# Optimization experiments

Measured on AMD Instinct MI355X. Metric: run time of the kernel, lower is better.

Reference implementation:

```python
import jax, jax.numpy as jnp
import numpy as np

B, S, H, D = 2, 2048, 16, 128
HID = H * D  # 2048


def _quantum(x, real, imag, phase, mag):
    # |x * e^{i*phase} * (real + i*imag) * mag| == |x| * sqrt(real^2+imag^2) * |mag|
    # (phase has unit modulus, so it drops out of the magnitude; grad wrt phase is 0,
    # matching torch.abs of the complex product.)
    return jnp.abs(x) * jnp.sqrt(real * real + imag * imag) * jnp.abs(mag)


def setup_inputs() -> dict:
    key = jax.random.key(0)
    ks = jax.random.split(key, 20)
    p = lambda i, shape, s=0.02: jax.random.normal(ks[i], shape, dtype=jnp.float32) * s
    inp = {
        "hidden_states": jax.random.normal(ks[0], (B, S, HID), dtype=jnp.float32),
        "attention_mask": jnp.zeros((B, 1, 1, S), dtype=jnp.float32),
    }
    i = 1
    for name in ("q", "k", "v"):
        inp[name + "_real"] = p(i, (HID,)); i += 1
        inp[name + "_imag"] = p(i, (HID,)); i += 1
        inp[name + "_phase"] = p(i, (HID,), 0.1); i += 1
        inp[name + "_mag"] = jnp.ones((HID,), dtype=jnp.float32)
    for name in ("q", "k", "v", "o"):
        inp["W" + name] = p(i, (HID, HID)); i += 1  # torch Linear weight [out, in]
        inp["b" + name] = jnp.zeros((HID,), dtype=jnp.float32)
    inp["ent"] = p(i, (H, H))
    return inp


def reference(hidden_states, attention_mask,
              q_real, q_imag, q_phase, q_mag,
              k_real, k_imag, k_phase, k_mag,
              v_real, v_imag, v_phase, v_mag,
              Wq, bq, Wk, bk, Wv, bv, Wo, bo, ent):
    Bsz, Sl, _ = hidden_states.shape

    def heads(x):  # [B,S,HID] -> [B,H,S,D]
        return x.reshape(Bsz, Sl, H, D).transpose(0, 2, 1, 3)

    q = heads(_quantum(hidden_states @ Wq.T + bq, q_real, q_imag, q_phase, q_mag))
    k = heads(_quantum(hidden_states @ Wk.T + bk, k_real, k_imag, k_phase, k_mag))
    v = heads(_quantum(hidden_states @ Wv.T + bv, v_real, v_imag, v_phase, v_mag))

    scores = jnp.einsum('bhsd,bhtd->bhst', q, k) / jnp.sqrt(jnp.float32(D))
    # entanglement bias: [H,H] tiled along key axis -> [1,H,1,S]
    bias = jnp.tile(ent, (1, Sl // H))[None, :, None, :]
    scores = scores + bias + attention_mask
    probs = jax.nn.softmax(scores, axis=-1)

    ctx = jnp.einsum('bhst,bhtd->bhsd', probs, v)
    ctx = ctx.transpose(0, 2, 1, 3).reshape(Bsz, Sl, HID)
    return ctx @ Wo.T + bo
```

## Files before the change

kernel.cpp:

```cpp
#include <hip/hip_runtime.h>
#include <hip/hip_bf16.h>

#define NB 2
#define NS 2048
#define NH 16
#define ND 128
#define HID2 2048
#define MROWS 4096

typedef __bf16 bf16;
typedef bf16 bf16x8 __attribute__((ext_vector_type(8)));
typedef bf16 bf16x4 __attribute__((ext_vector_type(4)));
typedef float f32x4 __attribute__((ext_vector_type(4)));
typedef unsigned int u32;

#define GLOBAL_AS __attribute__((address_space(1)))
#define LDS_AS __attribute__((address_space(3)))

__device__ __forceinline__ void async16(void* lds, const void* g) {
    __builtin_amdgcn_global_load_lds((const GLOBAL_AS u32*)g, (LDS_AS u32*)lds, 16, 0, 0);
}

__global__ void cvt_f32_bf16(const float* __restrict__ src, bf16* __restrict__ dst, int n8) {
    int i = blockIdx.x * blockDim.x + threadIdx.x;
    if (i >= n8) return;
    const float4* s4 = (const float4*)src;
    float4 a = s4[2 * i], b = s4[2 * i + 1];
    bf16x8 o;
    o[0] = (bf16)a.x; o[1] = (bf16)a.y; o[2] = (bf16)a.z; o[3] = (bf16)a.w;
    o[4] = (bf16)b.x; o[5] = (bf16)b.y; o[6] = (bf16)b.z; o[7] = (bf16)b.w;
    ((bf16x8*)dst)[i] = o;
}

__global__ void cvt_w4(const float* __restrict__ Wq, const float* __restrict__ Wk,
                       const float* __restrict__ Wv, const float* __restrict__ Wo,
                       bf16* __restrict__ dst) {
    int z = blockIdx.y;
    const float* src = (z == 0) ? Wq : (z == 1) ? Wk : (z == 2) ? Wv : Wo;
    int i = blockIdx.x * blockDim.x + threadIdx.x;
    const float4* s4 = (const float4*)src;
    float4 a = s4[2 * i], b = s4[2 * i + 1];
    bf16x8 o;
    o[0] = (bf16)a.x; o[1] = (bf16)a.y; o[2] = (bf16)a.z; o[3] = (bf16)a.w;
    o[4] = (bf16)b.x; o[5] = (bf16)b.y; o[6] = (bf16)b.z; o[7] = (bf16)b.w;
    ((bf16x8*)(dst + (size_t)z * HID2 * HID2))[i] = o;
}

__global__ void qscale_kernel(const float* qr, const float* qi, const float* qm,
                              const float* kr, const float* ki, const float* km,
                              const float* vr, const float* vi, const float* vm,
                              float* out) {
    int i = blockIdx.x * blockDim.x + threadIdx.x;
    if (i >= HID2) return;
    out[i]            = sqrtf(qr[i] * qr[i] + qi[i] * qi[i]) * fabsf(qm[i]);
    out[HID2 + i]     = sqrtf(kr[i] * kr[i] + ki[i] * ki[i]) * fabsf(km[i]);
    out[2 * HID2 + i] = sqrtf(vr[i] * vr[i] + vi[i] * vi[i]) * fabsf(vm[i]);
}

__device__ __forceinline__ void stage6(const char* gA, const char* gB,
                                       char* sa, char* sb, int w, int lane) {
#pragma unroll
    for (int j = 0; j < 2; ++j) {
        int r = w * 16 + j * 8 + (lane >> 3);
        async16(sa + (w * 16 + j * 8) * 128,
                gA + (size_t)r * (HID2 * 2) + (((lane & 7) * 16) ^ ((r & 7) << 4)));
    }
#pragma unroll
    for (int j = 0; j < 4; ++j) {
        int r = w * 32 + j * 8 + (lane >> 3);
        async16(sb + (w * 32 + j * 8) * 128,
                gB + (size_t)r * (HID2 * 2) + (((lane & 7) * 16) ^ ((r & 7) << 4)));
    }
}

template <int MODE>
__device__ __forceinline__ void gemm8_core(const bf16* __restrict__ A, const bf16* __restrict__ Bt,
                                           const float* __restrict__ bias, const float* __restrict__ scale,
                                           void* __restrict__ Cout, int tm, int tn) {
    __shared__ bf16 sA[3][128 * 64];
    __shared__ bf16 sB[3][256 * 64];
    const int NT = HID2 / 64;
    int tid = threadIdx.x, w = tid >> 6, lane = tid & 63;
    int wr = w >> 2, wc = w & 3;
    int l15 = lane & 15, l4 = lane >> 4;
    int xorb = (l15 & 7) << 4;

    const char* gAb = (const char*)(A + (size_t)tm * 128 * HID2);
    const char* gBb = (const char*)(Bt + (size_t)tn * 256 * HID2);

    f32x4 acc[4][4] = {};

    stage6(gAb, gBb, (char*)sA[0], (char*)sB[0], w, lane);
    stage6(gAb + 128, gBb + 128, (char*)sA[1], (char*)sB[1], w, lane);
    asm volatile("s_waitcnt vmcnt(6)" ::: "memory");
    __builtin_amdgcn_s_barrier();
    asm volatile("" ::: "memory");

    int cur = 0, nxt = 2;
    for (int t = 0; t < NT; ++t) {
        const char* pa = (const char*)sA[cur];
        const char* pb = (const char*)sB[cur];
        if (t + 2 < NT)
            stage6(gAb + (size_t)(t + 2) * 128, gBb + (size_t)(t + 2) * 128,
                   (char*)sA[nxt], (char*)sB[nxt], w, lane);
#pragma unroll
        for (int kk = 0; kk < 2; ++kk) {
            bf16x8 af[4], bg[4];
#pragma unroll
            for (int m = 0; m < 4; ++m)
                af[m] = *(const bf16x8*)(pa + (wr * 64 + m * 16 + l15) * 128 + ((kk * 64 + l4 * 16) ^ xorb));
#pragma unroll
            for (int n = 0; n < 4; ++n)
                bg[n] = *(const bf16x8*)(pb + (wc * 64 + n * 16 + l15) * 128 + ((kk * 64 + l4 * 16) ^ xorb));
#pragma unroll
            for (int m = 0; m < 4; ++m)
#pragma unroll
                for (int n = 0; n < 4; ++n)
                    acc[m][n] = __builtin_amdgcn_mfma_f32_16x16x32_bf16(af[m], bg[n], acc[m][n], 0, 0, 0);
        }
        if (t + 2 < NT)       { asm volatile("s_waitcnt vmcnt(6)" ::: "memory"); }
        else if (t + 2 == NT) { asm volatile("s_waitcnt vmcnt(0)" ::: "memory"); }
        if (t + 1 < NT) {
            __builtin_amdgcn_s_barrier();
            asm volatile("" ::: "memory");
        }
        cur = (cur == 2) ? 0 : cur + 1;
        nxt = (nxt == 2) ? 0 : nxt + 1;
    }

#pragma unroll
    for (int n = 0; n < 4; ++n) {
        int col = tn * 256 + wc * 64 + n * 16 + l15;
        float bv = bias[col];
        float sc = (MODE == 0) ? scale[col] : 0.f;
#pragma unroll
        for (int m = 0; m < 4; ++m) {
            int row = tm * 128 + wr * 64 + m * 16 + l4 * 4;
            if (MODE == 0) {
                bf16* Cp = (bf16*)Cout;
#pragma unroll
                for (int r = 0; r < 4; ++r)
                    Cp[(size_t)(row + r) * HID2 + col] = (bf16)(fabsf(acc[m][n][r] + bv) * sc);
            } else {
                float* Cp = (float*)Cout;
#pragma unroll
                for (int r = 0; r < 4; ++r)
                    Cp[(size_t)(row + r) * HID2 + col] = acc[m][n][r] + bv;
            }
        }
    }
}

__global__ __launch_bounds__(512, 2) void gemm8_qkv(
    const bf16* __restrict__ X, const bf16* __restrict__ Wb,
    const float* __restrict__ bq, const float* __restrict__ bk, const float* __restrict__ bv,
    const float* __restrict__ scales, bf16* __restrict__ QKV) {
    int z = blockIdx.y;
    int bid = blockIdx.x;
    int tn = bid & 7, tm = bid >> 3;
    const bf16* W = Wb + (size_t)z * HID2 * HID2;
    const float* bias = (z == 0) ? bq : (z == 1) ? bk : bv;
    gemm8_core<0>(X, W, bias, scales + z * HID2, QKV + (size_t)z * MROWS * HID2, tm, tn);
}

__global__ __launch_bounds__(512, 2) void gemm8_out(
    const bf16* __restrict__ Ctx, const bf16* __restrict__ Wo,
    const float* __restrict__ bo, float* __restrict__ out) {
    int bid = blockIdx.x;
    int tn = bid & 7, tm = bid >> 3;
    gemm8_core<1>(Ctx, Wo, bo, nullptr, out, tm, tn);
}

__global__ void transpose_v(const bf16* __restrict__ Vb, bf16* __restrict__ Vt) {
    int bh = blockIdx.z;
    int b = bh >> 4, h = bh & 15;
    int s0 = blockIdx.x * 64, d0 = blockIdx.y * 64;
    int tid = threadIdx.x;
    __shared__ bf16 T[64][72];
    const bf16* src = Vb + ((size_t)b * NS + s0) * HID2 + h * ND + d0;
#pragma unroll
    for (int i = 0; i < 2; ++i) {
        int r = i * 32 + (tid >> 3);
        int c = (tid & 7) * 8;
        *(bf16x8*)(&T[r][c]) = *(const bf16x8*)(src + (size_t)r * HID2 + c);
    }
    __syncthreads();
    bf16* dst = Vt + ((size_t)(b * NH + h) * ND + d0) * NS + s0;
#pragma unroll
    for (int i = 0; i < 2; ++i) {
        int dr = i * 32 + (tid >> 3);
        int sc = (tid & 7) * 8;
        bf16x8 o;
#pragma unroll
        for (int j = 0; j < 8; ++j) o[j] = T[sc + j][dr];
        *(bf16x8*)(dst + (size_t)dr * NS + sc) = o;
    }
}

__device__ __forceinline__ void stage_load(const bf16* __restrict__ Kp, const bf16* __restrict__ Vp,
                                           int kt, int tid, bf16x8 kreg[4], bf16x8 vreg[4]) {
#pragma unroll
    for (int i = 0; i < 4; ++i) {
        kreg[i] = *(const bf16x8*)(Kp + (size_t)(kt * 64 + i * 16 + (tid >> 4)) * HID2 + (tid & 15) * 8);
        vreg[i] = *(const bf16x8*)(Vp + (size_t)(i * 32 + (tid >> 3)) * NS + kt * 64 + (tid & 7) * 8);
    }
}

__global__ __launch_bounds__(256, 2) void flash_kernel(
    const bf16* __restrict__ Qb, const bf16* __restrict__ Kb, const bf16* __restrict__ Vt,
    const float* __restrict__ ent, const float* __restrict__ mask, bf16* __restrict__ Ctx) {
    int qt = blockIdx.x;
    int bh = blockIdx.y;
    int b = bh >> 4, h = bh & 15;
    int tid = threadIdx.x, wid = tid >> 6, lane = tid & 63;
    int l15 = lane & 15, l4 = lane >> 4;

    __shared__ bf16 Ks[64 * 136];
    __shared__ bf16 Vs[128 * 72];
    __shared__ bf16 Ps[4][32 * 72];

    const bf16* Qp = Qb + ((size_t)b * NS + qt * 128) * HID2 + h * ND;
    const bf16* Kp = Kb + (size_t)b * NS * HID2 + h * ND;
    const bf16* Vp = Vt + (size_t)(b * NH + h) * ND * NS;
    const float* maskp = mask + (size_t)b * NS;

    bf16x8 qf[2][4];
#pragma unroll
    for (int m = 0; m < 2; ++m)
#pragma unroll
        for (int kk = 0; kk < 4; ++kk)
            qf[m][kk] = *(const bf16x8*)(Qp + (size_t)(wid * 32 + m * 16 + l15) * HID2 + kk * 32 + l4 * 8);

    float eb[4];
#pragma unroll
    for (int r = 0; r < 4; ++r) eb[r] = ent[h * NH + l4 * 4 + r];
    const float RSQD = 0.08838834764831845f;

    float mrun[2], lrun[2];
    mrun[0] = mrun[1] = -INFINITY;
    lrun[0] = lrun[1] = 0.f;
    f32x4 oacc[2][8] = {};

    bf16x8 kreg[4], vreg[4];
    stage_load(Kp, Vp, 0, tid, kreg, vreg);
#pragma unroll
    for (int i = 0; i < 4; ++i) {
        *(bf16x8*)(&Ks[(i * 16 + (tid >> 4)) * 136 + (tid & 15) * 8]) = kreg[i];
        *(bf16x8*)(&Vs[(i * 32 + (tid >> 3)) * 72 + (tid & 7) * 8]) = vreg[i];
    }

    for (int kt = 0; kt < NS / 64; ++kt) {
        __syncthreads();
        if (kt + 1 < NS / 64) stage_load(Kp, Vp, kt + 1, tid, kreg, vreg);

        f32x4 s[2][4] = {};
#pragma unroll
        for (int kk = 0; kk < 4; ++kk) {
            bf16x8 kf[4];
#pragma unroll
            for (int n = 0; n < 4; ++n)
                kf[n] = *(const bf16x8*)(&Ks[(n * 16 + l15) * 136 + kk * 32 + l4 * 8]);
#pragma unroll
            for (int m = 0; m < 2; ++m)
#pragma unroll
                for (int n = 0; n < 4; ++n)
                    s[m][n] = __builtin_amdgcn_mfma_f32_16x16x32_bf16(kf[n], qf[m][kk], s[m][n], 0, 0, 0);
        }

        float4 mk[4];
#pragma unroll
        for (int n = 0; n < 4; ++n)
            mk[n] = *(const float4*)(maskp + kt * 64 + n * 16 + l4 * 4);

#pragma unroll
        for (int mq = 0; mq < 2; ++mq) {
            float sv[4][4];
#pragma unroll
            for (int n = 0; n < 4; ++n) {
                sv[n][0] = s[mq][n][0] * RSQD + eb[0] + mk[n].x;
                sv[n][1] = s[mq][n][1] * RSQD + eb[1] + mk[n].y;
                sv[n][2] = s[mq][n][2] * RSQD + eb[2] + mk[n].z;
                sv[n][3] = s[mq][n][3] * RSQD + eb[3] + mk[n].w;
            }
            float tmax = sv[0][0];
#pragma unroll
            for (int n = 0; n < 4; ++n)
#pragma unroll
                for (int r = 0; r < 4; ++r) tmax = fmaxf(tmax, sv[n][r]);
            tmax = fmaxf(tmax, __shfl_xor(tmax, 16));
            tmax = fmaxf(tmax, __shfl_xor(tmax, 32));

            if (__any(tmax > mrun[mq] + 8.0f)) {
                float mnew = fmaxf(mrun[mq], tmax);
                float corr = __expf(mrun[mq] - mnew);
                mrun[mq] = mnew;
                lrun[mq] *= corr;
#pragma unroll
                for (int r = 0; r < 4; ++r) {
                    float cr = __shfl(corr, l4 * 4 + r);
#pragma unroll
                    for (int n = 0; n < 8; ++n) oacc[mq][n][r] *= cr;
                }
            }

            float psum = 0.f;
#pragma unroll
            for (int n = 0; n < 4; ++n) {
                bf16x4 pv;
#pragma unroll
                for (int r = 0; r < 4; ++r) {
                    float p = __expf(sv[n][r] - mrun[mq]);
                    psum += p;
                    pv[r] = (bf16)p;
                }
                *(bf16x4*)(&Ps[wid][(mq * 16 + l15) * 72 + n * 16 + l4 * 4]) = pv;
            }
            psum += __shfl_xor(psum, 16);
            psum += __shfl_xor(psum, 32);
            lrun[mq] += psum;
        }

#pragma unroll
        for (int kk = 0; kk < 2; ++kk) {
            bf16x8 pa[2], vb[8];
#pragma unroll
            for (int m = 0; m < 2; ++m)
                pa[m] = *(const bf16x8*)(&Ps[wid][(m * 16 + l15) * 72 + kk * 32 + l4 * 8]);
#pragma unroll
            for (int n = 0; n < 8; ++n)
                vb[n] = *(const bf16x8*)(&Vs[(n * 16 + l15) * 72 + kk * 32 + l4 * 8]);
#pragma unroll
            for (int m = 0; m < 2; ++m)
#pragma unroll
                for (int n = 0; n < 8; ++n)
                    oacc[m][n] = __builtin_amdgcn_mfma_f32_16x16x32_bf16(pa[m], vb[n], oacc[m][n], 0, 0, 0);
        }
        __syncthreads();
        if (kt + 1 < NS / 64) {
#pragma unroll
            for (int i = 0; i < 4; ++i) {
                *(bf16x8*)(&Ks[(i * 16 + (tid >> 4)) * 136 + (tid & 15) * 8]) = kreg[i];
                *(bf16x8*)(&Vs[(i * 32 + (tid >> 3)) * 72 + (tid & 7) * 8]) = vreg[i];
            }
        }
    }

#pragma unroll
    for (int m = 0; m < 2; ++m) {
        float inv = 1.0f / lrun[m];
        float invr[4];
#pragma unroll
        for (int r = 0; r < 4; ++r) invr[r] = __shfl(inv, l4 * 4 + r);
#pragma unroll
        for (int r = 0; r < 4; ++r) {
            int row = qt * 128 + wid * 32 + m * 16 + l4 * 4 + r;
            bf16* Cp = Ctx + ((size_t)b * NS + row) * HID2 + h * ND;
#pragma unroll
            for (int n = 0; n < 8; ++n)
                Cp[n * 16 + l15] = (bf16)(oacc[m][n][r] * invr[r]);
        }
    }
}

extern "C" void kernel_launch(void* const* d_in, const int* in_sizes, int n_in,
                              void* d_out, int out_size, void* d_ws, size_t ws_size,
                              hipStream_t stream) {
    const float* hidden = (const float*)d_in[0];
    const float* mask   = (const float*)d_in[1];
    const float* q_real = (const float*)d_in[2];
    const float* q_imag = (const float*)d_in[3];
    const float* q_mag  = (const float*)d_in[5];
    const float* k_real = (const float*)d_in[6];
    const float* k_imag = (const float*)d_in[7];
    const float* k_mag  = (const float*)d_in[9];
    const float* v_real = (const float*)d_in[10];
    const float* v_imag = (const float*)d_in[11];
    const float* v_mag  = (const float*)d_in[13];
    const float* Wq = (const float*)d_in[14];
    const float* bq = (const float*)d_in[15];
    const float* Wk = (const float*)d_in[16];
    const float* bk = (const float*)d_in[17];
    const float* Wv = (const float*)d_in[18];
    const float* bv = (const float*)d_in[19];
    const float* Wo = (const float*)d_in[20];
    const float* bo = (const float*)d_in[21];
    const float* ent = (const float*)d_in[22];

    char* ws = (char*)d_ws;
    bf16* Xb    = (bf16*)(ws);
    bf16* Wb    = (bf16*)(ws + 16777216);
    bf16* Wob   = (bf16*)(ws + 41943040);
    bf16* QKV   = (bf16*)(ws + 50331648);
    bf16* Vt    = (bf16*)(ws + 100663296);
    bf16* Ctx   = (bf16*)(ws + 117440512);
    float* scales = (float*)(ws + 134217728);

    cvt_f32_bf16<<<4096, 256, 0, stream>>>(hidden, Xb, MROWS * HID2 / 8);
    cvt_w4<<<dim3(2048, 4), 256, 0, stream>>>(Wq, Wk, Wv, Wo, Wb);
    qscale_kernel<<<8, 256, 0, stream>>>(q_real, q_imag, q_mag, k_real, k_imag, k_mag,
                                         v_real, v_imag, v_mag, scales);
    gemm8_qkv<<<dim3(256, 3), 512, 0, stream>>>(Xb, Wb, bq, bk, bv, scales, QKV);
    const bf16* Vb = QKV + (size_t)2 * MROWS * HID2;
    transpose_v<<<dim3(32, 2, 32), 256, 0, stream>>>(Vb, Vt);
    flash_kernel<<<dim3(16, 32), 256, 0, stream>>>(QKV, QKV + (size_t)MROWS * HID2, Vt, ent, mask, Ctx);
    gemm8_out<<<256, 512, 0, stream>>>(Ctx, Wob, bo, (float*)d_out);
}
```

Baseline: 319.2 us.

## Enlarge GEMM tiles to 256x256 with double-buffered, barrier-phased MFMA schedule

```diff
diff --git a/kernel.cpp b/kernel.cpp
--- a/kernel.cpp
+++ b/kernel.cpp
@@ -57,75 +57,120 @@
     out[2 * HID2 + i] = sqrtf(vr[i] * vr[i] + vi[i] * vi[i]) * fabsf(vm[i]);
 }
 
-__device__ __forceinline__ void stage6(const char* gA, const char* gB,
-                                       char* sa, char* sb, int w, int lane) {
-#pragma unroll
-    for (int j = 0; j < 2; ++j) {
-        int r = w * 16 + j * 8 + (lane >> 3);
-        async16(sa + (w * 16 + j * 8) * 128,
-                gA + (size_t)r * (HID2 * 2) + (((lane & 7) * 16) ^ ((r & 7) << 4)));
-    }
+__device__ __forceinline__ void stage16(const char* gA, const char* gB, char* sa, char* sb,
+                                        int w, int lane, size_t kb) {
 #pragma unroll
     for (int j = 0; j < 4; ++j) {
-        int r = w * 32 + j * 8 + (lane >> 3);
-        async16(sb + (w * 32 + j * 8) * 128,
-                gB + (size_t)r * (HID2 * 2) + (((lane & 7) * 16) ^ ((r & 7) << 4)));
-    }
-}
+        int r = j * 64 + w * 8 + (lane >> 3);
+        async16(sa + (j * 64 + w * 8) * 128,
+                gA + (size_t)r * (HID2 * 2) + kb + (((lane & 7) * 16) ^ ((r & 7) << 4)));
+    }
+#pragma unroll
+    for (int j = 0; j < 4; ++j) {
+        int r = j * 64 + w * 8 + (lane >> 3);
+        async16(sb + (j * 64 + w * 8) * 128,
+                gB + (size_t)r * (HID2 * 2) + kb + (((lane & 7) * 16) ^ ((r & 7) << 4)));
+    }
+}
+
+#define G_BARRIER() do { asm volatile("" ::: "memory"); __builtin_amdgcn_s_barrier(); \
+                         asm volatile("" ::: "memory"); } while (0)
 
 template <int MODE>
-__device__ __forceinline__ void gemm8_core(const bf16* __restrict__ A, const bf16* __restrict__ Bt,
-                                           const float* __restrict__ bias, const float* __restrict__ scale,
-                                           void* __restrict__ Cout, int tm, int tn) {
-    __shared__ bf16 sA[3][128 * 64];
-    __shared__ bf16 sB[3][256 * 64];
+__device__ __forceinline__ void gemm256_core(const bf16* __restrict__ A, const bf16* __restrict__ Bt,
+                                             const float* __restrict__ bias, const float* __restrict__ scale,
+                                             void* __restrict__ Cout, int tm, int tn) {
+    __shared__ bf16 sA[2][256 * 64];
+    __shared__ bf16 sB[2][256 * 64];
     const int NT = HID2 / 64;
     int tid = threadIdx.x, w = tid >> 6, lane = tid & 63;
     int wr = w >> 2, wc = w & 3;
     int l15 = lane & 15, l4 = lane >> 4;
     int xorb = (l15 & 7) << 4;
-
-    const char* gAb = (const char*)(A + (size_t)tm * 128 * HID2);
-    const char* gBb = (const char*)(Bt + (size_t)tn * 256 * HID2);
-
-    f32x4 acc[4][4] = {};
-
-    stage6(gAb, gBb, (char*)sA[0], (char*)sB[0], w, lane);
-    stage6(gAb + 128, gBb + 128, (char*)sA[1], (char*)sB[1], w, lane);
-    asm volatile("s_waitcnt vmcnt(6)" ::: "memory");
-    __builtin_amdgcn_s_barrier();
-    asm volatile("" ::: "memory");
-
-    int cur = 0, nxt = 2;
+    int kc0 = (l4 * 16) ^ xorb;
+    int kc1 = (64 + l4 * 16) ^ xorb;
+    int arow = wr * 128 + l15;
+    int brow = wc * 64 + l15;
+
+    const char* gA = (const char*)A + (size_t)tm * 256 * (HID2 * 2);
+    const char* gB = (const char*)Bt + (size_t)tn * 256 * (HID2 * 2);
+
+    f32x4 acc[8][4] = {};
+
+    stage16(gA, gB, (char*)sA[0], (char*)sB[0], w, lane, 0);
+    asm volatile("s_waitcnt vmcnt(0)" ::: "memory");
+    G_BARRIER();
+
+    int cur = 0;
     for (int t = 0; t < NT; ++t) {
         const char* pa = (const char*)sA[cur];
         const char* pb = (const char*)sB[cur];
-        if (t + 2 < NT)
-            stage6(gAb + (size_t)(t + 2) * 128, gBb + (size_t)(t + 2) * 128,
-                   (char*)sA[nxt], (char*)sB[nxt], w, lane);
-#pragma unroll
-        for (int kk = 0; kk < 2; ++kk) {
-            bf16x8 af[4], bg[4];
-#pragma unroll
-            for (int m = 0; m < 4; ++m)
-                af[m] = *(const bf16x8*)(pa + (wr * 64 + m * 16 + l15) * 128 + ((kk * 64 + l4 * 16) ^ xorb));
-#pragma unroll
-            for (int n = 0; n < 4; ++n)
-                bg[n] = *(const bf16x8*)(pb + (wc * 64 + n * 16 + l15) * 128 + ((kk * 64 + l4 * 16) ^ xorb));
-#pragma unroll
-            for (int m = 0; m < 4; ++m)
-#pragma unroll
-                for (int n = 0; n < 4; ++n)
-                    acc[m][n] = __builtin_amdgcn_mfma_f32_16x16x32_bf16(af[m], bg[n], acc[m][n], 0, 0, 0);
-        }
-        if (t + 2 < NT)       { asm volatile("s_waitcnt vmcnt(6)" ::: "memory"); }
-        else if (t + 2 == NT) { asm volatile("s_waitcnt vmcnt(0)" ::: "memory"); }
-        if (t + 1 < NT) {
-            __builtin_amdgcn_s_barrier();
-            asm volatile("" ::: "memory");
-        }
-        cur = (cur == 2) ? 0 : cur + 1;
-        nxt = (nxt == 2) ? 0 : nxt + 1;
+        const bool pre = (t + 1 < NT);
+        bf16x8 af[4], bg[4];
+
+#pragma unroll
+        for (int n = 0; n < 4; ++n) bg[n] = *(const bf16x8*)(pb + (brow + n * 16) * 128 + kc0);
+#pragma unroll
+        for (int m = 0; m < 4; ++m) af[m] = *(const bf16x8*)(pa + (arow + m * 16) * 128 + kc0);
+        if (pre) stage16(gA, gB, (char*)sA[cur ^ 1], (char*)sB[cur ^ 1], w, lane, (size_t)(t + 1) * 128);
+        G_BARRIER();
+        asm volatile("s_waitcnt lgkmcnt(0)" ::: "memory");
+        __builtin_amdgcn_sched_barrier(0);
+        __builtin_amdgcn_s_setprio(1);
+#pragma unroll
+        for (int m = 0; m < 4; ++m)
+#pragma unroll
+            for (int n = 0; n < 4; ++n)
+                acc[m][n] = __builtin_amdgcn_mfma_f32_16x16x32_bf16(af[m], bg[n], acc[m][n], 0, 0, 0);
+        __builtin_amdgcn_s_setprio(0);
+        G_BARRIER();
+
+#pragma unroll
+        for (int m = 0; m < 4; ++m) af[m] = *(const bf16x8*)(pa + (arow + 64 + m * 16) * 128 + kc0);
+        G_BARRIER();
+        asm volatile("s_waitcnt lgkmcnt(0)" ::: "memory");
+        __builtin_amdgcn_sched_barrier(0);
+        __builtin_amdgcn_s_setprio(1);
+#pragma unroll
+        for (int m = 0; m < 4; ++m)
+#pragma unroll
+            for (int n = 0; n < 4; ++n)
+                acc[4 + m][n] = __builtin_amdgcn_mfma_f32_16x16x32_bf16(af[m], bg[n], acc[4 + m][n], 0, 0, 0);
+        __builtin_amdgcn_s_setprio(0);
+        G_BARRIER();
+
+#pragma unroll
+        for (int n = 0; n < 4; ++n) bg[n] = *(const bf16x8*)(pb + (brow + n * 16) * 128 + kc1);
+#pragma unroll
+        for (int m = 0; m < 4; ++m) af[m] = *(const bf16x8*)(pa + (arow + m * 16) * 128 + kc1);
+        G_BARRIER();
+        asm volatile("s_waitcnt lgkmcnt(0)" ::: "memory");
+        __builtin_amdgcn_sched_barrier(0);
+        __builtin_amdgcn_s_setprio(1);
+#pragma unroll
+        for (int m = 0; m < 4; ++m)
+#pragma unroll
+            for (int n = 0; n < 4; ++n)
+                acc[m][n] = __builtin_amdgcn_mfma_f32_16x16x32_bf16(af[m], bg[n], acc[m][n], 0, 0, 0);
+        __builtin_amdgcn_s_setprio(0);
+        G_BARRIER();
+
+#pragma unroll
+        for (int m = 0; m < 4; ++m) af[m] = *(const bf16x8*)(pa + (arow + 64 + m * 16) * 128 + kc1);
+        G_BARRIER();
+        asm volatile("s_waitcnt lgkmcnt(0)" ::: "memory");
+        __builtin_amdgcn_sched_barrier(0);
+        __builtin_amdgcn_s_setprio(1);
+#pragma unroll
+        for (int m = 0; m < 4; ++m)
+#pragma unroll
+            for (int n = 0; n < 4; ++n)
+                acc[4 + m][n] = __builtin_amdgcn_mfma_f32_16x16x32_bf16(af[m], bg[n], acc[4 + m][n], 0, 0, 0);
+        __builtin_amdgcn_s_setprio(0);
+        if (pre) { asm volatile("s_waitcnt vmcnt(0)" ::: "memory"); }
+        G_BARRIER();
+
+        cur ^= 1;
     }
 
 #pragma unroll
@@ -134,8 +179,8 @@
         float bv = bias[col];
         float sc = (MODE == 0) ? scale[col] : 0.f;
 #pragma unroll
-        for (int m = 0; m < 4; ++m) {
-            int row = tm * 128 + wr * 64 + m * 16 + l4 * 4;
+        for (int m = 0; m < 8; ++m) {
+            int row = tm * 256 + wr * 128 + m * 16 + l4 * 4;
             if (MODE == 0) {
                 bf16* Cp = (bf16*)Cout;
 #pragma unroll
@@ -151,24 +196,25 @@
     }
 }
 
-__global__ __launch_bounds__(512, 2) void gemm8_qkv(
+__global__ __launch_bounds__(512, 2) void gemm256_qkv(
     const bf16* __restrict__ X, const bf16* __restrict__ Wb,
     const float* __restrict__ bq, const float* __restrict__ bk, const float* __restrict__ bv,
     const float* __restrict__ scales, bf16* __restrict__ QKV) {
-    int z = blockIdx.y;
     int bid = blockIdx.x;
-    int tn = bid & 7, tm = bid >> 3;
+    int tng = (bid & 7) + (bid >> 7) * 8;
+    int tm = (bid >> 3) & 15;
+    int z = tng >> 3, tn = tng & 7;
     const bf16* W = Wb + (size_t)z * HID2 * HID2;
     const float* bias = (z == 0) ? bq : (z == 1) ? bk : bv;
-    gemm8_core<0>(X, W, bias, scales + z * HID2, QKV + (size_t)z * MROWS * HID2, tm, tn);
-}
-
-__global__ __launch_bounds__(512, 2) void gemm8_out(
+    gemm256_core<0>(X, W, bias, scales + z * HID2, QKV + (size_t)z * MROWS * HID2, tm, tn);
+}
+
+__global__ __launch_bounds__(512, 2) void gemm256_out(
     const bf16* __restrict__ Ctx, const bf16* __restrict__ Wo,
     const float* __restrict__ bo, float* __restrict__ out) {
     int bid = blockIdx.x;
     int tn = bid & 7, tm = bid >> 3;
-    gemm8_core<1>(Ctx, Wo, bo, nullptr, out, tm, tn);
+    gemm256_core<1>(Ctx, Wo, bo, nullptr, out, tm, tn);
 }
 
 __global__ void transpose_v(const bf16* __restrict__ Vb, bf16* __restrict__ Vt) {
@@ -399,9 +445,9 @@
     cvt_w4<<<dim3(2048, 4), 256, 0, stream>>>(Wq, Wk, Wv, Wo, Wb);
     qscale_kernel<<<8, 256, 0, stream>>>(q_real, q_imag, q_mag, k_real, k_imag, k_mag,
                                          v_real, v_imag, v_mag, scales);
-    gemm8_qkv<<<dim3(256, 3), 512, 0, stream>>>(Xb, Wb, bq, bk, bv, scales, QKV);
+    gemm256_qkv<<<384, 512, 0, stream>>>(Xb, Wb, bq, bk, bv, scales, QKV);
     const bf16* Vb = QKV + (size_t)2 * MROWS * HID2;
     transpose_v<<<dim3(32, 2, 32), 256, 0, stream>>>(Vb, Vt);
     flash_kernel<<<dim3(16, 32), 256, 0, stream>>>(QKV, QKV + (size_t)MROWS * HID2, Vt, ent, mask, Ctx);
-    gemm8_out<<<256, 512, 0, stream>>>(Ctx, Wob, bo, (float*)d_out);
-}
+    gemm256_out<<<128, 512, 0, stream>>>(Ctx, Wob, bo, (float*)d_out);
+}
```

Result: slower. 339.8 us (+6.5%).

## Replace triple-buffered 8-wave GEMM with single-buffered 4-wave larger-per-warp tiles

Applied to the files above, without the earlier changes.

```diff
diff --git a/kernel.cpp b/kernel.cpp
--- a/kernel.cpp
+++ b/kernel.cpp
@@ -57,80 +57,75 @@
     out[2 * HID2 + i] = sqrtf(vr[i] * vr[i] + vi[i] * vi[i]) * fabsf(vm[i]);
 }
 
-__device__ __forceinline__ void stage6(const char* gA, const char* gB,
-                                       char* sa, char* sb, int w, int lane) {
-#pragma unroll
-    for (int j = 0; j < 2; ++j) {
-        int r = w * 16 + j * 8 + (lane >> 3);
-        async16(sa + (w * 16 + j * 8) * 128,
-                gA + (size_t)r * (HID2 * 2) + (((lane & 7) * 16) ^ ((r & 7) << 4)));
-    }
+__device__ __forceinline__ void stage12(const char* gA, const char* gB,
+                                        char* sa, char* sb, int w, int lane, size_t kb) {
+    int r8 = lane >> 3;
+    int cx = (lane & 7) * 16;
 #pragma unroll
     for (int j = 0; j < 4; ++j) {
-        int r = w * 32 + j * 8 + (lane >> 3);
-        async16(sb + (w * 32 + j * 8) * 128,
-                gB + (size_t)r * (HID2 * 2) + (((lane & 7) * 16) ^ ((r & 7) << 4)));
+        int r = w * 32 + j * 8 + r8;
+        async16(sa + (w * 32 + j * 8) * 128,
+                gA + (size_t)r * (HID2 * 2) + kb + (cx ^ ((r & 7) << 4)));
+    }
+#pragma unroll
+    for (int j = 0; j < 8; ++j) {
+        int r = w * 64 + j * 8 + r8;
+        async16(sb + (w * 64 + j * 8) * 128,
+                gB + (size_t)r * (HID2 * 2) + kb + (cx ^ ((r & 7) << 4)));
     }
 }
 
 template <int MODE>
-__device__ __forceinline__ void gemm8_core(const bf16* __restrict__ A, const bf16* __restrict__ Bt,
-                                           const float* __restrict__ bias, const float* __restrict__ scale,
-                                           void* __restrict__ Cout, int tm, int tn) {
-    __shared__ bf16 sA[3][128 * 64];
-    __shared__ bf16 sB[3][256 * 64];
-    const int NT = HID2 / 64;
+__device__ __forceinline__ void gemm_core(const bf16* __restrict__ A, const bf16* __restrict__ Bt,
+                                          const float* __restrict__ bias, const float* __restrict__ scale,
+                                          void* __restrict__ Cout, int tm, int tn) {
+    __shared__ bf16 sA[128 * 64];
+    __shared__ bf16 sB[256 * 64];
     int tid = threadIdx.x, w = tid >> 6, lane = tid & 63;
-    int wr = w >> 2, wc = w & 3;
+    int wr = w >> 1, wc = w & 1;
     int l15 = lane & 15, l4 = lane >> 4;
     int xorb = (l15 & 7) << 4;
 
-    const char* gAb = (const char*)(A + (size_t)tm * 128 * HID2);
-    const char* gBb = (const char*)(Bt + (size_t)tn * 256 * HID2);
-
-    f32x4 acc[4][4] = {};
-
-    stage6(gAb, gBb, (char*)sA[0], (char*)sB[0], w, lane);
-    stage6(gAb + 128, gBb + 128, (char*)sA[1], (char*)sB[1], w, lane);
-    asm volatile("s_waitcnt vmcnt(6)" ::: "memory");
-    __builtin_amdgcn_s_barrier();
-    asm volatile("" ::: "memory");
-
-    int cur = 0, nxt = 2;
-    for (int t = 0; t < NT; ++t) {
-        const char* pa = (const char*)sA[cur];
-        const char* pb = (const char*)sB[cur];
-        if (t + 2 < NT)
-            stage6(gAb + (size_t)(t + 2) * 128, gBb + (size_t)(t + 2) * 128,
-                   (char*)sA[nxt], (char*)sB[nxt], w, lane);
+    const char* gA = (const char*)A + (size_t)tm * 128 * (HID2 * 2);
+    const char* gB = (const char*)Bt + (size_t)tn * 256 * (HID2 * 2);
+    const char* pa = (const char*)sA;
+    const char* pb = (const char*)sB;
+
+    f32x4 acc[4][8] = {};
+
+    for (int t = 0; t < HID2 / 64; ++t) {
+        stage12(gA, gB, (char*)sA, (char*)sB, w, lane, (size_t)t * 128);
+        __syncthreads();
 #pragma unroll
         for (int kk = 0; kk < 2; ++kk) {
+            int kc = (kk * 64 + l4 * 16) ^ xorb;
             bf16x8 af[4], bg[4];
 #pragma unroll
             for (int m = 0; m < 4; ++m)
-                af[m] = *(const bf16x8*)(pa + (wr * 64 + m * 16 + l15) * 128 + ((kk * 64 + l4 * 16) ^ xorb));
+                af[m] = *(const bf16x8*)(pa + (wr * 64 + m * 16 + l15) * 128 + kc);
 #pragma unroll
             for (int n = 0; n < 4; ++n)
-                bg[n] = *(const bf16x8*)(pb + (wc * 64 + n * 16 + l15) * 128 + ((kk * 64 + l4 * 16) ^ xorb));
+                bg[n] = *(const bf16x8*)(pb + (wc * 128 + n * 16 + l15) * 128 + kc);
 #pragma unroll
             for (int m = 0; m < 4; ++m)
 #pragma unroll
                 for (int n = 0; n < 4; ++n)
                     acc[m][n] = __builtin_amdgcn_mfma_f32_16x16x32_bf16(af[m], bg[n], acc[m][n], 0, 0, 0);
-        }
-        if (t + 2 < NT)       { asm volatile("s_waitcnt vmcnt(6)" ::: "memory"); }
-        else if (t + 2 == NT) { asm volatile("s_waitcnt vmcnt(0)" ::: "memory"); }
-        if (t + 1 < NT) {
-            __builtin_amdgcn_s_barrier();
-            asm volatile("" ::: "memory");
-        }
-        cur = (cur == 2) ? 0 : cur + 1;
-        nxt = (nxt == 2) ? 0 : nxt + 1;
-    }
-
-#pragma unroll
-    for (int n = 0; n < 4; ++n) {
-        int col = tn * 256 + wc * 64 + n * 16 + l15;
+#pragma unroll
+            for (int n = 0; n < 4; ++n)
+                bg[n] = *(const bf16x8*)(pb + (wc * 128 + (n + 4) * 16 + l15) * 128 + kc);
+#pragma unroll
+            for (int m = 0; m < 4; ++m)
+#pragma unroll
+                for (int n = 0; n < 4; ++n)
+                    acc[m][n + 4] = __builtin_amdgcn_mfma_f32_16x16x32_bf16(af[m], bg[n], acc[m][n + 4], 0, 0, 0);
+        }
+        __syncthreads();
+    }
+
+#pragma unroll
+    for (int n = 0; n < 8; ++n) {
+        int col = tn * 256 + wc * 128 + n * 16 + l15;
         float bv = bias[col];
         float sc = (MODE == 0) ? scale[col] : 0.f;
 #pragma unroll
@@ -151,24 +146,24 @@
     }
 }
 
-__global__ __launch_bounds__(512, 2) void gemm8_qkv(
+__global__ __launch_bounds__(256, 2) void gemm_qkv(
     const bf16* __restrict__ X, const bf16* __restrict__ Wb,
     const float* __restrict__ bq, const float* __restrict__ bk, const float* __restrict__ bv,
     const float* __restrict__ scales, bf16* __restrict__ QKV) {
-    int z = blockIdx.y;
     int bid = blockIdx.x;
-    int tn = bid & 7, tm = bid >> 3;
+    int p = bid & 7, q = bid >> 3;
+    int z = q >> 5, tm = q & 31, tn = p;
     const bf16* W = Wb + (size_t)z * HID2 * HID2;
     const float* bias = (z == 0) ? bq : (z == 1) ? bk : bv;
-    gemm8_core<0>(X, W, bias, scales + z * HID2, QKV + (size_t)z * MROWS * HID2, tm, tn);
-}
-
-__global__ __launch_bounds__(512, 2) void gemm8_out(
+    gemm_core<0>(X, W, bias, scales + z * HID2, QKV + (size_t)z * MROWS * HID2, tm, tn);
+}
+
+__global__ __launch_bounds__(256, 2) void gemm_out(
     const bf16* __restrict__ Ctx, const bf16* __restrict__ Wo,
     const float* __restrict__ bo, float* __restrict__ out) {
     int bid = blockIdx.x;
     int tn = bid & 7, tm = bid >> 3;
-    gemm8_core<1>(Ctx, Wo, bo, nullptr, out, tm, tn);
+    gemm_core<1>(Ctx, Wo, bo, nullptr, out, tm, tn);
 }
 
 __global__ void transpose_v(const bf16* __restrict__ Vb, bf16* __restrict__ Vt) {
@@ -399,9 +394,9 @@
     cvt_w4<<<dim3(2048, 4), 256, 0, stream>>>(Wq, Wk, Wv, Wo, Wb);
     qscale_kernel<<<8, 256, 0, stream>>>(q_real, q_imag, q_mag, k_real, k_imag, k_mag,
                                          v_real, v_imag, v_mag, scales);
-    gemm8_qkv<<<dim3(256, 3), 512, 0, stream>>>(Xb, Wb, bq, bk, bv, scales, QKV);
+    gemm_qkv<<<768, 256, 0, stream>>>(Xb, Wb, bq, bk, bv, scales, QKV);
     const bf16* Vb = QKV + (size_t)2 * MROWS * HID2;
     transpose_v<<<dim3(32, 2, 32), 256, 0, stream>>>(Vb, Vt);
     flash_kernel<<<dim3(16, 32), 256, 0, stream>>>(QKV, QKV + (size_t)MROWS * HID2, Vt, ent, mask, Ctx);
-    gemm8_out<<<256, 512, 0, stream>>>(Ctx, Wob, bo, (float*)d_out);
-}
+    gemm_out<<<256, 256, 0, stream>>>(Ctx, Wob, bo, (float*)d_out);
+}
```

Measured after the change: 311.2 us. 1.03x faster.

## Split GEMM k-tile into ping-pong halves with interleaved prefetch and setprio

Applied to the files above, without the earlier changes.

```diff
diff --git a/kernel.cpp b/kernel.cpp
--- a/kernel.cpp
+++ b/kernel.cpp
@@ -57,26 +57,30 @@
     out[2 * HID2 + i] = sqrtf(vr[i] * vr[i] + vi[i] * vi[i]) * fabsf(vm[i]);
 }
 
-__device__ __forceinline__ void stage6(const char* gA, const char* gB,
-                                       char* sa, char* sb, int w, int lane) {
+__device__ __forceinline__ void stage2A(const char* gA, char* sa, int w, int lane, size_t kb) {
 #pragma unroll
     for (int j = 0; j < 2; ++j) {
         int r = w * 16 + j * 8 + (lane >> 3);
         async16(sa + (w * 16 + j * 8) * 128,
-                gA + (size_t)r * (HID2 * 2) + (((lane & 7) * 16) ^ ((r & 7) << 4)));
-    }
-#pragma unroll
-    for (int j = 0; j < 4; ++j) {
-        int r = w * 32 + j * 8 + (lane >> 3);
-        async16(sb + (w * 32 + j * 8) * 128,
-                gB + (size_t)r * (HID2 * 2) + (((lane & 7) * 16) ^ ((r & 7) << 4)));
-    }
-}
+                gA + (size_t)r * (HID2 * 2) + kb + (((lane & 7) * 16) ^ ((r & 7) << 4)));
+    }
+}
+__device__ __forceinline__ void stage2B(const char* gB, char* sb, int w, int lane, int half, size_t kb) {
+#pragma unroll
+    for (int j = 0; j < 2; ++j) {
+        int r = half * 128 + w * 16 + j * 8 + (lane >> 3);
+        async16(sb + (half * 128 + w * 16 + j * 8) * 128,
+                gB + (size_t)r * (HID2 * 2) + kb + (((lane & 7) * 16) ^ ((r & 7) << 4)));
+    }
+}
+
+#define G_BARRIER() do { asm volatile("" ::: "memory"); __builtin_amdgcn_s_barrier(); \
+                         asm volatile("" ::: "memory"); } while (0)
 
 template <int MODE>
-__device__ __forceinline__ void gemm8_core(const bf16* __restrict__ A, const bf16* __restrict__ Bt,
-                                           const float* __restrict__ bias, const float* __restrict__ scale,
-                                           void* __restrict__ Cout, int tm, int tn) {
+__device__ __forceinline__ void gemm_core(const bf16* __restrict__ A, const bf16* __restrict__ Bt,
+                                          const float* __restrict__ bias, const float* __restrict__ scale,
+                                          void* __restrict__ Cout, int tm, int tn) {
     __shared__ bf16 sA[3][128 * 64];
     __shared__ bf16 sB[3][256 * 64];
     const int NT = HID2 / 64;
@@ -85,47 +89,76 @@
     int l15 = lane & 15, l4 = lane >> 4;
     int xorb = (l15 & 7) << 4;
 
-    const char* gAb = (const char*)(A + (size_t)tm * 128 * HID2);
-    const char* gBb = (const char*)(Bt + (size_t)tn * 256 * HID2);
+    const char* gA = (const char*)A + (size_t)tm * 128 * (HID2 * 2);
+    const char* gB = (const char*)Bt + (size_t)tn * 256 * (HID2 * 2);
 
     f32x4 acc[4][4] = {};
 
-    stage6(gAb, gBb, (char*)sA[0], (char*)sB[0], w, lane);
-    stage6(gAb + 128, gBb + 128, (char*)sA[1], (char*)sB[1], w, lane);
+    stage2A(gA, (char*)sA[0], w, lane, 0);
+    stage2B(gB, (char*)sB[0], w, lane, 0, 0);
+    stage2B(gB, (char*)sB[0], w, lane, 1, 0);
+    stage2A(gA, (char*)sA[1], w, lane, 128);
+    stage2B(gB, (char*)sB[1], w, lane, 0, 128);
+    stage2B(gB, (char*)sB[1], w, lane, 1, 128);
     asm volatile("s_waitcnt vmcnt(6)" ::: "memory");
-    __builtin_amdgcn_s_barrier();
-    asm volatile("" ::: "memory");
-
-    int cur = 0, nxt = 2;
+    G_BARRIER();
+
+    int cur = 0;
     for (int t = 0; t < NT; ++t) {
         const char* pa = (const char*)sA[cur];
         const char* pb = (const char*)sB[cur];
-        if (t + 2 < NT)
-            stage6(gAb + (size_t)(t + 2) * 128, gBb + (size_t)(t + 2) * 128,
-                   (char*)sA[nxt], (char*)sB[nxt], w, lane);
-#pragma unroll
-        for (int kk = 0; kk < 2; ++kk) {
-            bf16x8 af[4], bg[4];
+        int nb = cur + 2; if (nb >= 3) nb -= 3;
+        const bool pre = (t + 2 < NT);
+        size_t kb = (size_t)(t + 2) * 128;
+        bf16x8 af[4], bg[4];
+
+        {
+            int kc = (l4 * 16) ^ xorb;
 #pragma unroll
             for (int m = 0; m < 4; ++m)
-                af[m] = *(const bf16x8*)(pa + (wr * 64 + m * 16 + l15) * 128 + ((kk * 64 + l4 * 16) ^ xorb));
-#pragma unroll
-            for (int n = 0; n < 4; ++n)
-                bg[n] = *(const bf16x8*)(pb + (wc * 64 + n * 16 + l15) * 128 + ((kk * 64 + l4 * 16) ^ xorb));
+                af[m] = *(const bf16x8*)(pa + (wr * 64 + m * 16 + l15) * 128 + kc);
+#pragma unroll
+            for (int n = 0; n < 4; ++n)
+                bg[n] = *(const bf16x8*)(pb + (wc * 64 + n * 16 + l15) * 128 + kc);
+        }
+        if (pre) { stage2A(gA, (char*)sA[nb], w, lane, kb); stage2B(gB, (char*)sB[nb], w, lane, 0, kb); }
+        G_BARRIER();
+        asm volatile("s_waitcnt lgkmcnt(0)" ::: "memory");
+        __builtin_amdgcn_sched_barrier(0);
+        __builtin_amdgcn_s_setprio(1);
+#pragma unroll
+        for (int m = 0; m < 4; ++m)
+#pragma unroll
+            for (int n = 0; n < 4; ++n)
+                acc[m][n] = __builtin_amdgcn_mfma_f32_16x16x32_bf16(af[m], bg[n], acc[m][n], 0, 0, 0);
+        __builtin_amdgcn_s_setprio(0);
+        G_BARRIER();
+
+        {
+            int kc = (64 + l4 * 16) ^ xorb;
 #pragma unroll
             for (int m = 0; m < 4; ++m)
-#pragma unroll
-                for (int n = 0; n < 4; ++n)
-                    acc[m][n] = __builtin_amdgcn_mfma_f32_16x16x32_bf16(af[m], bg[n], acc[m][n], 0, 0, 0);
-        }
-        if (t + 2 < NT)       { asm volatile("s_waitcnt vmcnt(6)" ::: "memory"); }
-        else if (t + 2 == NT) { asm volatile("s_waitcnt vmcnt(0)" ::: "memory"); }
-        if (t + 1 < NT) {
-            __builtin_amdgcn_s_barrier();
-            asm volatile("" ::: "memory");
-        }
-        cur = (cur == 2) ? 0 : cur + 1;
-        nxt = (nxt == 2) ? 0 : nxt + 1;
+                af[m] = *(const bf16x8*)(pa + (wr * 64 + m * 16 + l15) * 128 + kc);
+#pragma unroll
+            for (int n = 0; n < 4; ++n)
+                bg[n] = *(const bf16x8*)(pb + (wc * 64 + n * 16 + l15) * 128 + kc);
+        }
+        if (pre) stage2B(gB, (char*)sB[nb], w, lane, 1, kb);
+        G_BARRIER();
+        asm volatile("s_waitcnt lgkmcnt(0)" ::: "memory");
+        __builtin_amdgcn_sched_barrier(0);
+        __builtin_amdgcn_s_setprio(1);
+#pragma unroll
+        for (int m = 0; m < 4; ++m)
+#pragma unroll
+            for (int n = 0; n < 4; ++n)
+                acc[m][n] = __builtin_amdgcn_mfma_f32_16x16x32_bf16(af[m], bg[n], acc[m][n], 0, 0, 0);
+        __builtin_amdgcn_s_setprio(0);
+        if (pre)                { asm volatile("s_waitcnt vmcnt(6)" ::: "memory"); }
+        else if (t + 2 == NT)  { asm volatile("s_waitcnt vmcnt(0)" ::: "memory"); }
+        G_BARRIER();
+
+        cur = cur + 1; if (cur == 3) cur = 0;
     }
 
 #pragma unroll
@@ -151,7 +184,7 @@
     }
 }
 
-__global__ __launch_bounds__(512, 2) void gemm8_qkv(
+__global__ __launch_bounds__(512, 2) void gemm_qkv(
     const bf16* __restrict__ X, const bf16* __restrict__ Wb,
     const float* __restrict__ bq, const float* __restrict__ bk, const float* __restrict__ bv,
     const float* __restrict__ scales, bf16* __restrict__ QKV) {
@@ -160,15 +193,15 @@
     int tn = bid & 7, tm = bid >> 3;
     const bf16* W = Wb + (size_t)z * HID2 * HID2;
     const float* bias = (z == 0) ? bq : (z == 1) ? bk : bv;
-    gemm8_core<0>(X, W, bias, scales + z * HID2, QKV + (size_t)z * MROWS * HID2, tm, tn);
-}
-
-__global__ __launch_bounds__(512, 2) void gemm8_out(
+    gemm_core<0>(X, W, bias, scales + z * HID2, QKV + (size_t)z * MROWS * HID2, tm, tn);
+}
+
+__global__ __launch_bounds__(512, 2) void gemm_out(
     const bf16* __restrict__ Ctx, const bf16* __restrict__ Wo,
     const float* __restrict__ bo, float* __restrict__ out) {
     int bid = blockIdx.x;
     int tn = bid & 7, tm = bid >> 3;
-    gemm8_core<1>(Ctx, Wo, bo, nullptr, out, tm, tn);
+    gemm_core<1>(Ctx, Wo, bo, nullptr, out, tm, tn);
 }
 
 __global__ void transpose_v(const bf16* __restrict__ Vb, bf16* __restrict__ Vt) {
@@ -399,9 +432,9 @@
     cvt_w4<<<dim3(2048, 4), 256, 0, stream>>>(Wq, Wk, Wv, Wo, Wb);
     qscale_kernel<<<8, 256, 0, stream>>>(q_real, q_imag, q_mag, k_real, k_imag, k_mag,
                                          v_real, v_imag, v_mag, scales);
-    gemm8_qkv<<<dim3(256, 3), 512, 0, stream>>>(Xb, Wb, bq, bk, bv, scales, QKV);
+    gemm_qkv<<<dim3(256, 3), 512, 0, stream>>>(Xb, Wb, bq, bk, bv, scales, QKV);
     const bf16* Vb = QKV + (size_t)2 * MROWS * HID2;
     transpose_v<<<dim3(32, 2, 32), 256, 0, stream>>>(Vb, Vt);
     flash_kernel<<<dim3(16, 32), 256, 0, stream>>>(QKV, QKV + (size_t)MROWS * HID2, Vt, ent, mask, Ctx);
-    gemm8_out<<<256, 512, 0, stream>>>(Ctx, Wob, bo, (float*)d_out);
-}
+    gemm_out<<<256, 512, 0, stream>>>(Ctx, Wob, bo, (float*)d_out);
+}
```

Result: faster. 290.5 us (-9.0%).
